# Optimization experiments

Measured on AMD Instinct MI355X. Metric: run time of the kernel, lower is better.

The kernel has to match this reference:

```python
import math
import jax, jax.numpy as jnp
import numpy as np

B, CIN, Hh, Ww = 8, 3, 64, 64
D_MODEL = 512
N_STATE = 64
N2 = N_STATE // 2
N_LAYERS = 4
LATENT = 256
L = Hh * Ww  # 4096
EPS = 1e-5


def setup_inputs() -> dict:
    key = jax.random.key(0)
    ks = jax.random.split(key, 12)
    x = jax.random.normal(ks[0], (B, CIN, Hh, Ww), jnp.float32)
    Wproj = jax.random.normal(ks[1], (D_MODEL, CIN), jnp.float32) * (1.0 / math.sqrt(CIN))
    bproj = jnp.zeros((D_MODEL,), jnp.float32)
    pos_emb = jax.random.normal(ks[2], (1, L, D_MODEL), jnp.float32)
    # S4D kernel params (stacked over layers), per minimal S4D init
    log_dt = jax.random.uniform(ks[3], (N_LAYERS, D_MODEL), jnp.float32) * (math.log(0.1) - math.log(0.001)) + math.log(0.001)
    log_A_real = jnp.full((N_LAYERS, D_MODEL, N2), math.log(0.5), jnp.float32)
    A_imag = jnp.broadcast_to(math.pi * jnp.arange(N2, dtype=jnp.float32), (N_LAYERS, D_MODEL, N2)) + jnp.zeros((N_LAYERS, D_MODEL, N2), jnp.float32)
    C_re = jax.random.normal(ks[4], (N_LAYERS, D_MODEL, N2), jnp.float32) * (0.5 ** 0.5)
    C_im = jax.random.normal(ks[5], (N_LAYERS, D_MODEL, N2), jnp.float32) * (0.5 ** 0.5)
    Dskip = jax.random.normal(ks[6], (N_LAYERS, D_MODEL), jnp.float32)
    Wout = jax.random.normal(ks[7], (N_LAYERS, 2 * D_MODEL, D_MODEL), jnp.float32) * (1.0 / math.sqrt(D_MODEL))
    bout = jnp.zeros((N_LAYERS, 2 * D_MODEL), jnp.float32)
    ln_g = jnp.ones((N_LAYERS, D_MODEL), jnp.float32)
    ln_b = jnp.zeros((N_LAYERS, D_MODEL), jnp.float32)
    Wstats = jax.random.normal(ks[8], (2 * LATENT, D_MODEL), jnp.float32) * (1.0 / math.sqrt(D_MODEL))
    bstats = jnp.zeros((2 * LATENT,), jnp.float32)
    return dict(x=x, Wproj=Wproj, bproj=bproj, pos_emb=pos_emb, log_dt=log_dt,
                log_A_real=log_A_real, A_imag=A_imag, C_re=C_re, C_im=C_im,
                Dskip=Dskip, Wout=Wout, bout=bout, ln_g=ln_g, ln_b=ln_b,
                Wstats=Wstats, bstats=bstats)


def _s4d_layer(u, log_dt, log_A_real, A_imag, C_re, C_im, Dskip, Wout, bout):
    # u: (B, H, L); diagonal SSM via Vandermonde kernel + FFT conv (minimal S4D)
    Lseq = u.shape[-1]
    dt = jnp.exp(log_dt)                              # (H,)
    A = -jnp.exp(log_A_real) + 1j * A_imag            # (H, N2)
    dtA = A * dt[:, None]                             # (H, N2)
    Cc = (C_re + 1j * C_im) * (jnp.exp(dtA) - 1.0) / A
    t = jnp.arange(Lseq, dtype=jnp.float32)
    K = 2.0 * jnp.einsum('hn,hnl->hl', Cc, jnp.exp(dtA[:, :, None] * t)).real  # (H, L)
    k_f = jnp.fft.rfft(K, n=2 * Lseq)                 # (H, L+1)
    u_f = jnp.fft.rfft(u, n=2 * Lseq)                 # (B, H, L+1)
    y = jnp.fft.irfft(u_f * k_f, n=2 * Lseq)[..., :Lseq]
    y = y + u * Dskip[:, None]
    y = jax.nn.gelu(y, approximate=False)
    # 1x1 conv to 2H then GLU over channel dim
    y2 = jnp.einsum('oh,bhl->bol', Wout, y) + bout[:, None]
    a, b = jnp.split(y2, 2, axis=1)
    return a * jax.nn.sigmoid(b)


def _layernorm(x, g, b):
    # x: (B, L, H), normalize over H
    mu = jnp.mean(x, axis=-1, keepdims=True)
    var = jnp.mean((x - mu) ** 2, axis=-1, keepdims=True)
    return (x - mu) * jax.lax.rsqrt(var + EPS) * g + b


def reference(x, Wproj, bproj, pos_emb, log_dt, log_A_real, A_imag, C_re, C_im,
              Dskip, Wout, bout, ln_g, ln_b, Wstats, bstats):
    Bx = x.shape[0]
    # 1x1 Conv2d input projection
    h = jnp.einsum('oc,bchw->bohw', Wproj, x) + bproj[None, :, None, None]
    h = h.reshape(Bx, D_MODEL, L).transpose(0, 2, 1)  # (B, L, D)
    h = h + pos_emb
    h = h.transpose(0, 2, 1)                          # (B, D, L)
    for i in range(N_LAYERS):
        z = _s4d_layer(h, log_dt[i], log_A_real[i], A_imag[i], C_re[i], C_im[i],
                       Dskip[i], Wout[i], bout[i])
        h = h + z                                     # residual (dropout = identity at eval)
        h = _layernorm(h.transpose(0, 2, 1), ln_g[i], ln_b[i]).transpose(0, 2, 1)
    h = h.mean(-1)                                    # (B, D)
    stats = h @ Wstats.T + bstats
    mu, log_sig = jnp.split(stats, 2, axis=-1)
    return mu, log_sig
```

## Files before the change

### kernel.cpp

```cpp
#include <hip/hip_runtime.h>
#include <hip/hip_bf16.h>
#include <hip/hip_fp16.h>
#include <cmath>

#define BATCH   8
#define D_MODEL 512
#define N2      32
#define LSEQ    4096
#define NLAYERS 4
#define CIN     3
#define NBDL    (16777216u)
#define PN      (D_MODEL * N2)
#define WN      (2 * D_MODEL * D_MODEL)

typedef __attribute__((ext_vector_type(8))) short short8;
typedef __attribute__((ext_vector_type(4))) float floatx4;

__device__ float   g_h[NBDL];
__device__ __align__(16) __hip_bfloat16 g_yb[NBDL];
__device__ __align__(16) __hip_bfloat16 g_yt[NBDL];
__device__ __align__(16) __hip_bfloat16 g_wb[NLAYERS * WN];
__device__ __align__(16) __hip_bfloat16 g_G[(size_t)NLAYERS * 512 * 6 * 4096];
__device__ float4  g_p[NLAYERS * PN];
__device__ float   g_hm[BATCH * D_MODEL];
__device__ int     g_flag;

__device__ __forceinline__ float bfbits2f(unsigned short u) {
    union { unsigned int i; float f; } x; x.i = ((unsigned int)u) << 16; return x.f;
}
__device__ __forceinline__ float halfbits2f(unsigned short u) {
    __half h; *(unsigned short*)&h = u; return __half2float(h);
}
__device__ __forceinline__ float ldin(const void* p, size_t i, int m) {
    if (m == 1) return ((const float*)p)[i];
    unsigned short u = ((const unsigned short*)p)[i];
    if (m == 0) return bfbits2f(u);
    return halfbits2f(u);
}
__device__ __forceinline__ unsigned int pk2(float a, float b) {
    __hip_bfloat16 ha = __float2bfloat16(a), hb = __float2bfloat16(b);
    unsigned short ua, ub;
    __builtin_memcpy(&ua, &ha, 2); __builtin_memcpy(&ub, &hb, 2);
    return (unsigned int)ua | ((unsigned int)ub << 16);
}
__device__ __forceinline__ void split2(float a, float b, unsigned int& hp, unsigned int& lp) {
    __hip_bfloat16 ah = __float2bfloat16(a), bh = __float2bfloat16(b);
    unsigned short ua, ub;
    __builtin_memcpy(&ua, &ah, 2); __builtin_memcpy(&ub, &bh, 2);
    hp = (unsigned int)ua | ((unsigned int)ub << 16);
    lp = pk2(a - __bfloat162float(ah), b - __bfloat162float(bh));
}
__device__ __forceinline__ float2 cpow_(float br, float bi, int e) {
    float rr = 1.f, ri = 0.f;
    while (e) {
        if (e & 1) { float t = rr * br - ri * bi; ri = rr * bi + ri * br; rr = t; }
        float t = br * br - bi * bi; bi = 2.f * br * bi; br = t;
        e >>= 1;
    }
    return make_float2(rr, ri);
}

__device__ __forceinline__ float fast_gelu(float x) {
    float z = x * 0.70710678118654752f;
    float a = fabsf(z);
    float t = __builtin_amdgcn_rcpf(fmaf(0.3275911f, a, 1.0f));
    float p = t * fmaf(t, fmaf(t, fmaf(t, fmaf(t, 1.061405429f, -1.453152027f),
                                       1.421413741f), -0.284496736f), 0.254829592f);
    float e = __expf(-a * a);
    float er = fmaf(-p, e, 1.0f);
    er = copysignf(er, z);
    float hx = 0.5f * x;
    return fmaf(hx, er, hx);
}

__global__ void detect_kernel(const unsigned short* a) {
    if (threadIdx.x == 0) {
        unsigned short h1 = a[1], h3 = a[3];
        int f;
        if (h1 == 0x0000 && h3 == 0x4049) f = 1;
        else if (h1 == 0x4049)            f = 0;
        else if (h1 == 0x4248)            f = 2;
        else                              f = 1;
        g_flag = f;
    }
}

__global__ __launch_bounds__(256) void sentinel_kernel(float* out, float v) {
    out[blockIdx.x * 256 + threadIdx.x] = v;
}

__global__ __launch_bounds__(256) void proj_kernel(const void* x, const void* Wproj,
                                                   const void* bproj, const void* pos) {
    const int m = g_flag;
    unsigned idx = blockIdx.x * 256 + threadIdx.x;
    int l = idx & (LSEQ - 1);
    int o = (idx >> 12) & (D_MODEL - 1);
    int b = idx >> 21;
    float acc = ldin(bproj, o, m) + ldin(pos, (size_t)l * D_MODEL + o, m);
#pragma unroll
    for (int c = 0; c < CIN; c++)
        acc = fmaf(ldin(Wproj, o * CIN + c, m),
                   ldin(x, (size_t)(b * CIN + c) * LSEQ + l, m), acc);
    g_h[idx] = acc;
}

__global__ __launch_bounds__(256) void prep_kernel(const void* log_dt, const void* log_A_real,
                                                   const void* A_imag, const void* C_re,
                                                   const void* C_im) {
    const int m = g_flag;
    int idx = blockIdx.x * 256 + threadIdx.x;
    int layer = idx >> 14;
    int i = idx & (PN - 1);
    int hh = i >> 5;
    size_t oH = (size_t)layer * D_MODEL;
    size_t oN = (size_t)layer * PN;
    float dt  = expf(ldin(log_dt, oH + hh, m));
    float a   = expf(ldin(log_A_real, oN + i, m));
    float bi  = ldin(A_imag, oN + i, m);
    float dre = -a * dt, dim = bi * dt;
    float er  = expf(dre);
    float wr  = er * cosf(dim);
    float wi  = er * sinf(dim);
    float Er  = wr - 1.0f, Ei = wi;
    float inv = 1.0f / (a * a + bi * bi);
    float Tr = (-Er * a + Ei * bi) * inv;
    float Ti = -(Er * bi + Ei * a) * inv;
    float cr = ldin(C_re, oN + i, m), ci = ldin(C_im, oN + i, m);
    float c2r = 2.0f * (cr * Tr - ci * Ti);
    float c2i = 2.0f * (cr * Ti + ci * Tr);
    g_p[idx] = make_float4(wr, wi, c2r, c2i);
}

__global__ __launch_bounds__(256) void pack_w_kernel(const void* Wout) {
    int idx = blockIdx.x * 256 + threadIdx.x;
    g_wb[idx] = __float2bfloat16(ldin(Wout, idx, g_flag));
}

__global__ __launch_bounds__(256) void gmat_kernel() {
    __shared__ float4 psh[32];
    __shared__ float Ksh[64];
    int tid = threadIdx.x;
    int bid = blockIdx.x;
    int layer = bid >> 9, h = bid & 511;
    if (tid < 32) psh[tid] = g_p[(size_t)layer * PN + h * N2 + tid];
    __syncthreads();
    if (tid < 64) {
        float acc = 0.f;
        for (int n = 0; n < 32; n++) {
            float4 pv = psh[n];
            float2 wd = cpow_(pv.x, pv.y, tid);
            acc = fmaf(pv.z, wd.x, fmaf(-pv.w, wd.y, acc));
        }
        Ksh[tid] = acc;
    }
    __syncthreads();
    __hip_bfloat16* G = g_G + (size_t)bid * 6 * 4096;
    for (int e = tid; e < 4096; e += 256) {
        int t = e >> 6, j = e & 63;
        float kv = (t >= j) ? Ksh[t - j] : 0.f;
        __hip_bfloat16 khi = __float2bfloat16(kv);
        G[e] = khi;
        G[4096 + e] = __float2bfloat16(kv - __bfloat162float(khi));
        {
            int n = t >> 1;
            float4 pv = psh[n];
            float2 wd = cpow_(pv.x, pv.y, 63 - j);
            float av = (t & 1) ? wd.y : wd.x;
            __hip_bfloat16 ahi = __float2bfloat16(av);
            G[2 * 4096 + e] = ahi;
            G[3 * 4096 + e] = __float2bfloat16(av - __bfloat162float(ahi));
        }
        {
            int n = j >> 1;
            float4 pv = psh[n];
            float2 wd = cpow_(pv.x, pv.y, t + 1);
            float zr = pv.z * wd.x - pv.w * wd.y;
            float zi = pv.z * wd.y + pv.w * wd.x;
            float cv = (j & 1) ? -zi : zr;
            __hip_bfloat16 chi = __float2bfloat16(cv);
            G[4 * 4096 + e] = chi;
            G[5 * 4096 + e] = __float2bfloat16(cv - __bfloat162float(chi));
        }
    }
}

__global__ __launch_bounds__(256) void ssd_kernel(const void* Dskip, int layer) {
    __shared__ unsigned short sMhi[64][72];
    __shared__ unsigned short sMlo[64][72];
    __shared__ unsigned short sAC[64][72];
    __shared__ unsigned short sUhi[64][72];
    __shared__ unsigned short sUlo[64][72];
    __shared__ float sPf[64][68];
    const int m = g_flag;
    int tid = threadIdx.x;
    int bid = blockIdx.x;
    int h = bid >> 3, b = bid & 7;
    const unsigned short* Gsrc = (const unsigned short*)g_G + (size_t)(layer * 512 + h) * 6 * 4096;

    {
        int row = tid >> 2, seg = (tid & 3) * 16;
        const unsigned short* s = Gsrc + row * 64 + seg;
        *(uint4*)&sMhi[row][seg]     = *(const uint4*)(s);
        *(uint4*)&sMhi[row][seg + 8] = *(const uint4*)(s + 8);
        *(uint4*)&sMlo[row][seg]     = *(const uint4*)(s + 4096);
        *(uint4*)&sMlo[row][seg + 8] = *(const uint4*)(s + 4096 + 8);
        *(uint4*)&sAC[row][seg]      = *(const uint4*)(s + 2 * 4096);
        *(uint4*)&sAC[row][seg + 8]  = *(const uint4*)(s + 2 * 4096 + 8);
    }
    {
        const float* ub = g_h + (size_t)(b * D_MODEL + h) * LSEQ;
        int c = tid >> 2, j0 = (tid & 3) * 16;
        const float* up = ub + c * 64 + j0;
#pragma unroll
        for (int s8 = 0; s8 < 2; s8++) {
            float4 va = *(const float4*)(up + s8 * 8);
            float4 vb = *(const float4*)(up + s8 * 8 + 4);
            uint4 H, L;
            split2(va.x, va.y, H.x, L.x);
            split2(va.z, va.w, H.y, L.y);
            split2(vb.x, vb.y, H.z, L.z);
            split2(vb.z, vb.w, H.w, L.w);
            *(uint4*)&sUhi[c][j0 + s8 * 8] = H;
            *(uint4*)&sUlo[c][j0 + s8 * 8] = L;
        }
    }
    __syncthreads();

    int lane = tid & 63, wave = tid >> 6;
    int q = lane >> 4, nm = lane & 15;
    int cidx = wave * 16 + nm;
    floatx4 zed = {0.f, 0.f, 0.f, 0.f};
    floatx4 pacc[4] = {zed, zed, zed, zed};

#pragma unroll
    for (int k0 = 0; k0 < 64; k0 += 32) {
        short8 bh = *(short8*)&sUhi[cidx][k0 + q * 8];
        short8 bl = *(short8*)&sUlo[cidx][k0 + q * 8];
#pragma unroll
        for (int mi = 0; mi < 4; mi++) {
            short8 a = *(short8*)&sAC[mi * 16 + nm][k0 + q * 8];
            pacc[mi] = __builtin_amdgcn_mfma_f32_16x16x32_bf16(a, bh, pacc[mi], 0, 0, 0);
            pacc[mi] = __builtin_amdgcn_mfma_f32_16x16x32_bf16(a, bl, pacc[mi], 0, 0, 0);
        }
    }
    __syncthreads();
    if (tid >= 128) {
        int idx = tid - 128, row = idx >> 1, seg = (idx & 1) * 32;
        const unsigned short* s = Gsrc + 3 * 4096 + row * 64 + seg;
        *(uint4*)&sAC[row][seg]      = *(const uint4*)(s);
        *(uint4*)&sAC[row][seg + 8]  = *(const uint4*)(s + 8);
        *(uint4*)&sAC[row][seg + 16] = *(const uint4*)(s + 16);
        *(uint4*)&sAC[row][seg + 24] = *(const uint4*)(s + 24);
    }
    __syncthreads();
#pragma unroll
    for (int k0 = 0; k0 < 64; k0 += 32) {
        short8 bh = *(short8*)&sUhi[cidx][k0 + q * 8];
#pragma unroll
        for (int mi = 0; mi < 4; mi++) {
            short8 a = *(short8*)&sAC[mi * 16 + nm][k0 + q * 8];
            pacc[mi] = __builtin_amdgcn_mfma_f32_16x16x32_bf16(a, bh, pacc[mi], 0, 0, 0);
        }
    }
#pragma unroll
    for (int mi = 0; mi < 4; mi++)
        *(floatx4*)&sPf[cidx][mi * 16 + q * 4] = pacc[mi];
    __syncthreads();

    if (tid < 32) {
        int n = tid;
        float4 pv = g_p[(size_t)layer * PN + h * N2 + n];
        float Wr = pv.x, Wi = pv.y;
#pragma unroll
        for (int s6 = 0; s6 < 6; s6++) { float t2 = Wr * Wr - Wi * Wi; Wi = 2.f * Wr * Wi; Wr = t2; }
        float Sr = 0.f, Si = 0.f;
        for (int c = 0; c < 64; c++) {
            unsigned int* wp = (unsigned int*)&sPf[c][0];
            unsigned int pru = wp[2 * n], piu = wp[2 * n + 1];
            float pr = __uint_as_float(pru), pi = __uint_as_float(piu);
            unsigned int shw, slw;
            split2(Sr, Si, shw, slw);
            wp[n]      = shw;
            wp[32 + n] = slw;
            float t2 = fmaf(Wr, Sr, fmaf(-Wi, Si, pr));
            Si = fmaf(Wr, Si, fmaf(Wi, Sr, pi));
            Sr = t2;
        }
    }
    if (tid >= 128) {
        int idx = tid - 128, row = idx >> 1, seg = (idx & 1) * 32;
        const unsigned short* s = Gsrc + 4 * 4096 + row * 64 + seg;
        *(uint4*)&sAC[row][seg]      = *(const uint4*)(s);
        *(uint4*)&sAC[row][seg + 8]  = *(const uint4*)(s + 8);
        *(uint4*)&sAC[row][seg + 16] = *(const uint4*)(s + 16);
        *(uint4*)&sAC[row][seg + 24] = *(const uint4*)(s + 24);
    }
    __syncthreads();

    floatx4 accA[4] = {zed, zed, zed, zed};
    floatx4 accB[4] = {zed, zed, zed, zed};
#pragma unroll
    for (int k0 = 0; k0 < 64; k0 += 32) {
        short8 bh = *(short8*)&sUhi[cidx][k0 + q * 8];
        short8 bl = *(short8*)&sUlo[cidx][k0 + q * 8];
        const unsigned short* srow = (const unsigned short*)&sPf[cidx][0];
        short8 sh = *(short8*)(srow + k0 + q * 8);
        short8 sl = *(short8*)(srow + 64 + k0 + q * 8);
#pragma unroll
        for (int mi = 0; mi < 4; mi++) {
            short8 amh = *(short8*)&sMhi[mi * 16 + nm][k0 + q * 8];
            short8 aml = *(short8*)&sMlo[mi * 16 + nm][k0 + q * 8];
            short8 ac  = *(short8*)&sAC [mi * 16 + nm][k0 + q * 8];
            accA[mi] = __builtin_amdgcn_mfma_f32_16x16x32_bf16(amh, bh, accA[mi], 0, 0, 0);
            accA[mi] = __builtin_amdgcn_mfma_f32_16x16x32_bf16(amh, bl, accA[mi], 0, 0, 0);
            accA[mi] = __builtin_amdgcn_mfma_f32_16x16x32_bf16(aml, bh, accA[mi], 0, 0, 0);
            accB[mi] = __builtin_amdgcn_mfma_f32_16x16x32_bf16(ac,  sh, accB[mi], 0, 0, 0);
            accB[mi] = __builtin_amdgcn_mfma_f32_16x16x32_bf16(ac,  sl, accB[mi], 0, 0, 0);
        }
    }
    __syncthreads();
    if (tid >= 128) {
        int idx = tid - 128, row = idx >> 1, seg = (idx & 1) * 32;
        const unsigned short* s = Gsrc + 5 * 4096 + row * 64 + seg;
        *(uint4*)&sAC[row][seg]      = *(const uint4*)(s);
        *(uint4*)&sAC[row][seg + 8]  = *(const uint4*)(s + 8);
        *(uint4*)&sAC[row][seg + 16] = *(const uint4*)(s + 16);
        *(uint4*)&sAC[row][seg + 24] = *(const uint4*)(s + 24);
    }
    __syncthreads();
#pragma unroll
    for (int k0 = 0; k0 < 64; k0 += 32) {
        const unsigned short* srow = (const unsigned short*)&sPf[cidx][0];
        short8 sh = *(short8*)(srow + k0 + q * 8);
#pragma unroll
        for (int mi = 0; mi < 4; mi++) {
            short8 ac = *(short8*)&sAC[mi * 16 + nm][k0 + q * 8];
            accB[mi] = __builtin_amdgcn_mfma_f32_16x16x32_bf16(ac, sh, accB[mi], 0, 0, 0);
        }
    }

    float dsk = ldin(Dskip, (size_t)layer * D_MODEL + h, m);
    __hip_bfloat16* yb = g_yb + (size_t)(b * D_MODEL + h) * LSEQ;
#pragma unroll
    for (int mi = 0; mi < 4; mi++) {
        int t0 = mi * 16 + q * 4;
        uint2 uh = *(uint2*)&sUhi[cidx][t0];
        uint2 ul = *(uint2*)&sUlo[cidx][t0];
        float u0 = bfbits2f((unsigned short)(uh.x & 0xFFFF)) + bfbits2f((unsigned short)(ul.x & 0xFFFF));
        float u1 = bfbits2f((unsigned short)(uh.x >> 16))    + bfbits2f((unsigned short)(ul.x >> 16));
        float u2 = bfbits2f((unsigned short)(uh.y & 0xFFFF)) + bfbits2f((unsigned short)(ul.y & 0xFFFF));
        float u3 = bfbits2f((unsigned short)(uh.y >> 16))    + bfbits2f((unsigned short)(ul.y >> 16));
        float y0 = fast_gelu(accA[mi][0] + accB[mi][0] + dsk * u0);
        float y1 = fast_gelu(accA[mi][1] + accB[mi][1] + dsk * u1);
        float y2 = fast_gelu(accA[mi][2] + accB[mi][2] + dsk * u2);
        float y3 = fast_gelu(accA[mi][3] + accB[mi][3] + dsk * u3);
        uint2 o;
        o.x = pk2(y0, y1);
        o.y = pk2(y2, y3);
        *(uint2*)&yb[cidx * 64 + t0] = o;
    }
}

__global__ __launch_bounds__(256, 4) void glu_mfma_kernel(const void* bout, int layer) {
    __shared__ __align__(16) unsigned char smem[25600];
    unsigned short (* __restrict__ Wa)[40] = (unsigned short(*)[40])(smem);
    unsigned short (* __restrict__ Wb)[40] = (unsigned short(*)[40])(smem + 2560);
    unsigned int*  __restrict__ Ytd        = (unsigned int*)(smem + 5120);
    unsigned short (* __restrict__ Zs)[264] = (unsigned short(*)[264])(smem);
    const int m = g_flag;
    int tid  = threadIdx.x;
    int wave = tid >> 6, lane = tid & 63;
    int q = lane >> 4, nm = lane & 15;
    int bid = blockIdx.x;
    int xcd = bid & 7;
    int qb  = bid >> 3;
    int rt  = qb & 15;
    int ct  = (xcd << 4) | (qb >> 4);
    int col0 = ct * 256;
    int row0 = rt * 32;
    int b  = col0 >> 12;
    int l0 = col0 & (LSEQ - 1);
    const unsigned short* __restrict__ Ybb =
        (const unsigned short*)g_yb + (size_t)b * D_MODEL * LSEQ;
    const __hip_bfloat16* __restrict__ Wbase = g_wb + (size_t)layer * WN;

    floatx4 accA[2][4], accB[2][4];
    floatx4 zed = {0.f, 0.f, 0.f, 0.f};
#pragma unroll
    for (int i = 0; i < 2; i++)
#pragma unroll
        for (int j = 0; j < 4; j++) { accA[i][j] = zed; accB[i][j] = zed; }

    int sk = (tid & 3) * 8;
    int wrow = (tid & 127) >> 2;
    int p  = tid >> 4;
    int sg = tid & 15;
    int Xw = (sg & 3) << 2;
    unsigned int rowbase = (unsigned)(sg * 16) * 20 + (unsigned)(p ^ Xw);
    int wavecol = wave * 64;

    for (int k0 = 0; k0 < D_MODEL; k0 += 32) {
        if (tid < 128)
            *(uint4*)&Wa[wrow][sk] = *(const uint4*)&Wbase[(size_t)(row0 + wrow) * D_MODEL + k0 + sk];
        else
            *(uint4*)&Wb[wrow][sk] = *(const uint4*)&Wbase[(size_t)(row0 + wrow + D_MODEL) * D_MODEL + k0 + sk];
        {
            const unsigned short* yA = Ybb + (size_t)(k0 + 2 * p) * LSEQ + l0 + sg * 16;
            uint4 a0 = *(const uint4*)yA;
            uint4 a1 = *(const uint4*)(yA + 8);
            uint4 b0 = *(const uint4*)(yA + LSEQ);
            uint4 b1 = *(const uint4*)(yA + LSEQ + 8);
#define PKW(au, bu, jj)  { \
            Ytd[rowbase + (jj) * 20]       = ((au) & 0xFFFFu) | ((bu) << 16); \
            Ytd[rowbase + ((jj) + 1) * 20] = ((au) >> 16) | ((bu) & 0xFFFF0000u); }
            PKW(a0.x, b0.x, 0)  PKW(a0.y, b0.y, 2)  PKW(a0.z, b0.z, 4)  PKW(a0.w, b0.w, 6)
            PKW(a1.x, b1.x, 8)  PKW(a1.y, b1.y, 10) PKW(a1.z, b1.z, 12) PKW(a1.w, b1.w, 14)
#undef PKW
        }
        __syncthreads();
        short8 afa[2], afb[2];
#pragma unroll
        for (int mi = 0; mi < 2; mi++) {
            afa[mi] = *(short8*)&Wa[mi * 16 + nm][q * 8];
            afb[mi] = *(short8*)&Wb[mi * 16 + nm][q * 8];
        }
#pragma unroll
        for (int ni = 0; ni < 4; ni++) {
            int r = wavecol + ni * 16 + nm;
            int Xr = ((r >> 4) & 3) << 2;
            short8 bf = *(short8*)(Ytd + r * 20 + ((q * 4) ^ Xr));
#pragma unroll
            for (int mi = 0; mi < 2; mi++) {
                accA[mi][ni] = __builtin_amdgcn_mfma_f32_16x16x32_bf16(afa[mi], bf, accA[mi][ni], 0, 0, 0);
                accB[mi][ni] = __builtin_amdgcn_mfma_f32_16x16x32_bf16(afb[mi], bf, accB[mi][ni], 0, 0, 0);
            }
        }
        __syncthreads();
    }

    size_t boff = (size_t)layer * 2 * D_MODEL;
#pragma unroll
    for (int mi = 0; mi < 2; mi++) {
#pragma unroll
        for (int r = 0; r < 4; r++) {
            int lrow = mi * 16 + q * 4 + r;
            int o = row0 + lrow;
            float ba  = ldin(bout, boff + o, m);
            float bb2 = ldin(bout, boff + o + D_MODEL, m);
#pragma unroll
            for (int ni = 0; ni < 4; ni++) {
                int lcol = wavecol + ni * 16 + nm;
                float aa = accA[mi][ni][r] + ba;
                float bv = accB[mi][ni][r] + bb2;
                float z  = aa * __builtin_amdgcn_rcpf(1.0f + __expf(-bv));
                __half hz = __float2half(z);
                unsigned short hzb;
                __builtin_memcpy(&hzb, &hz, 2);
                Zs[lrow][lcol] = hzb;
            }
        }
    }
    __syncthreads();
    unsigned short* __restrict__ Zb =
        (unsigned short*)g_yt + (size_t)b * D_MODEL * LSEQ;
    int zrow = tid >> 3;
    int zcol = (tid & 7) * 32;
    size_t gbase = (size_t)(row0 + zrow) * LSEQ + l0 + zcol;
#pragma unroll
    for (int i = 0; i < 4; i++)
        *(uint4*)&Zb[gbase + i * 8] = *(uint4*)&Zs[zrow][zcol + i * 8];
}

__global__ __launch_bounds__(256) void ln_kernel(const void* g, const void* bt, int layer) {
    __shared__ float s_sum[8][32];
    __shared__ float s_sq[8][32];
    __shared__ float s_mu[32], s_rs[32];
    const int m = g_flag;
    int tid = threadIdx.x;
    int l  = tid & 31;
    int dg = tid >> 5;
    int bl = blockIdx.x;
    int b  = bl >> 7;
    int l0 = (bl & 127) * 32;
    size_t base = (size_t)b * D_MODEL * LSEQ + l0 + l;
    float* __restrict__ hp = g_h + base + (size_t)(dg * 64) * LSEQ;
    const unsigned short* __restrict__ zp =
        (const unsigned short*)g_yt + base + (size_t)(dg * 64) * LSEQ;
    size_t goff = (size_t)layer * D_MODEL + dg * 64;
    float varr[64];
    float sum = 0.f, sq = 0.f;
#pragma unroll
    for (int i = 0; i < 64; i++) {
        float v = hp[(size_t)i * LSEQ] + halfbits2f(zp[(size_t)i * LSEQ]);
        varr[i] = v;
        sum += v; sq += v * v;
    }
    s_sum[dg][l] = sum; s_sq[dg][l] = sq;
    __syncthreads();
    if (tid < 32) {
        float s = 0.f, qq = 0.f;
#pragma unroll
        for (int gq = 0; gq < 8; gq++) { s += s_sum[gq][tid]; qq += s_sq[gq][tid]; }
        float mu = s * (1.0f / D_MODEL);
        float var = qq * (1.0f / D_MODEL) - mu * mu;
        s_mu[tid] = mu;
        s_rs[tid] = rsqrtf(var + 1e-5f);
    }
    __syncthreads();
    float mu = s_mu[l], rs = s_rs[l];
#pragma unroll
    for (int i = 0; i < 64; i++) {
        hp[(size_t)i * LSEQ] = (varr[i] - mu) * rs * ldin(g, goff + i, m) + ldin(bt, goff + i, m);
    }
}

__global__ __launch_bounds__(256) void mean_kernel() {
    int bd = blockIdx.x;
    int tid = threadIdx.x;
    const float* __restrict__ row = g_h + (size_t)bd * LSEQ;
    float s = 0.f;
    for (int l = tid; l < LSEQ; l += 256) s += row[l];
#pragma unroll
    for (int off = 32; off > 0; off >>= 1) s += __shfl_down(s, off, 64);
    __shared__ float red[4];
    if ((tid & 63) == 0) red[tid >> 6] = s;
    __syncthreads();
    if (tid == 0) g_hm[bd] = (red[0] + red[1] + red[2] + red[3]) * (1.0f / LSEQ);
}

__global__ __launch_bounds__(256) void stats_kernel(const void* Wst, const void* bst,
                                                    float* __restrict__ out) {
    const int m = g_flag;
    int idx = blockIdx.x * 256 + threadIdx.x;
    int b = idx >> 9, o = idx & (D_MODEL - 1);
    const float* __restrict__ hb = g_hm + b * D_MODEL;
    float acc = ldin(bst, o, m);
    for (int d = 0; d < D_MODEL; d++)
        acc = fmaf(hb[d], ldin(Wst, (size_t)o * D_MODEL + d, m), acc);
    int pos = (o < 256) ? (b * 256 + o) : (2048 + b * 256 + (o - 256));
    out[pos] = acc;
}

extern "C" void kernel_launch(void* const* d_in, const int* in_sizes, int n_in,
                              void* d_out, int out_size, void* d_ws, size_t ws_size,
                              hipStream_t stream) {
    static const int exp_sizes[16] = {98304, 1536, 512, 2097152, 2048, 65536, 65536,
                                      65536, 65536, 2048, 2097152, 4096, 2048, 2048,
                                      262144, 512};
    bool ok = (n_in == 16);
    if (ok) for (int i = 0; i < 16; i++) if (in_sizes[i] != exp_sizes[i]) { ok = false; break; }
    if (!ok) {
        sentinel_kernel<<<(out_size + 255) / 256, 256, 0, stream>>>((float*)d_out, 1000.0f);
        return;
    }
    if (out_size != 4096) {
        sentinel_kernel<<<(out_size + 255) / 256, 256, 0, stream>>>((float*)d_out, 300.0f);
        return;
    }

    const void* x          = d_in[0];
    const void* Wproj      = d_in[1];
    const void* bproj      = d_in[2];
    const void* pos        = d_in[3];
    const void* log_dt     = d_in[4];
    const void* log_A_real = d_in[5];
    const void* A_imag     = d_in[6];
    const void* C_re       = d_in[7];
    const void* C_im       = d_in[8];
    const void* Dskip      = d_in[9];
    const void* Wout       = d_in[10];
    const void* bout       = d_in[11];
    const void* ln_g       = d_in[12];
    const void* ln_b       = d_in[13];
    const void* Wstats     = d_in[14];
    const void* bstats     = d_in[15];

    detect_kernel<<<1, 64, 0, stream>>>((const unsigned short*)A_imag);
    proj_kernel<<<NBDL / 256, 256, 0, stream>>>(x, Wproj, bproj, pos);
    prep_kernel<<<(NLAYERS * PN) / 256, 256, 0, stream>>>(
        log_dt, log_A_real, A_imag, C_re, C_im);
    pack_w_kernel<<<(NLAYERS * WN) / 256, 256, 0, stream>>>(Wout);
    gmat_kernel<<<NLAYERS * 512, 256, 0, stream>>>();

    for (int i = 0; i < NLAYERS; i++) {
        ssd_kernel<<<BATCH * D_MODEL, 256, 0, stream>>>(Dskip, i);
        glu_mfma_kernel<<<2048, 256, 0, stream>>>(bout, i);
        ln_kernel<<<(BATCH * LSEQ) / 32, 256, 0, stream>>>(ln_g, ln_b, i);
    }

    mean_kernel<<<BATCH * D_MODEL, 256, 0, stream>>>();
    stats_kernel<<<(BATCH * D_MODEL) / 256, 256, 0, stream>>>(
        Wstats, bstats, (float*)d_out);
}
```

Baseline: 1.113 ms.

## Rewrite gmat kernel with incremental complex powers and vectorized stores; remap SSD blocks

Each gmat thread now computes a 16-element run with a single cpow_ call followed by repeated complex multiplication, replacing a binary-exponentiation call per element. The kernel K is built from per-mode partial sums staged in shared memory. The G matrices are written with 16-byte vector stores, and the transposed C block goes through shared memory so its global stores stay coalesced. The SSD block index mapping changes to h = bid & 511, b = bid >> 9, so consecutive blocks now take different heads; this alters how G reads hit the cache. Building powers by repeated multiplication accumulates a little more rounding error than direct exponentiation.

```diff
diff --git a/kernel.cpp b/kernel.cpp
--- a/kernel.cpp
+++ b/kernel.cpp
@@ -49,6 +49,10 @@
     __builtin_memcpy(&ua, &ah, 2); __builtin_memcpy(&ub, &bh, 2);
     hp = (unsigned int)ua | ((unsigned int)ub << 16);
     lp = pk2(a - __bfloat162float(ah), b - __bfloat162float(bh));
+}
+__device__ __forceinline__ unsigned short bf16u(float a) {
+    __hip_bfloat16 h = __float2bfloat16(a);
+    unsigned short u; __builtin_memcpy(&u, &h, 2); return u;
 }
 __device__ __forceinline__ float2 cpow_(float br, float bi, int e) {
     float rr = 1.f, ri = 0.f;
@@ -138,50 +142,110 @@
 
 __global__ __launch_bounds__(256) void gmat_kernel() {
     __shared__ float4 psh[32];
-    __shared__ float Ksh[64];
+    __shared__ unsigned short Khi[64], Klo[64];
+    __shared__ __align__(16) unsigned short sC[2][64][72];
+    float (*Kpart)[64] = (float(*)[64])&sC[0][0][0];
     int tid = threadIdx.x;
     int bid = blockIdx.x;
     int layer = bid >> 9, h = bid & 511;
     if (tid < 32) psh[tid] = g_p[(size_t)layer * PN + h * N2 + tid];
     __syncthreads();
+    if (tid < 128) {
+        int n = tid >> 2, dseg = (tid & 3) * 16;
+        float4 pv = psh[n];
+        float wr = pv.x, wi = pv.y;
+        float2 wd = cpow_(wr, wi, dseg);
+#pragma unroll
+        for (int i = 0; i < 16; i++) {
+            Kpart[n][dseg + i] = pv.z * wd.x - pv.w * wd.y;
+            float t2 = wd.x * wr - wd.y * wi;
+            wd.y = wd.x * wi + wd.y * wr; wd.x = t2;
+        }
+    }
+    __syncthreads();
     if (tid < 64) {
         float acc = 0.f;
-        for (int n = 0; n < 32; n++) {
-            float4 pv = psh[n];
-            float2 wd = cpow_(pv.x, pv.y, tid);
-            acc = fmaf(pv.z, wd.x, fmaf(-pv.w, wd.y, acc));
-        }
-        Ksh[tid] = acc;
-    }
-    __syncthreads();
-    __hip_bfloat16* G = g_G + (size_t)bid * 6 * 4096;
-    for (int e = tid; e < 4096; e += 256) {
-        int t = e >> 6, j = e & 63;
-        float kv = (t >= j) ? Ksh[t - j] : 0.f;
-        __hip_bfloat16 khi = __float2bfloat16(kv);
-        G[e] = khi;
-        G[4096 + e] = __float2bfloat16(kv - __bfloat162float(khi));
-        {
-            int n = t >> 1;
-            float4 pv = psh[n];
-            float2 wd = cpow_(pv.x, pv.y, 63 - j);
-            float av = (t & 1) ? wd.y : wd.x;
-            __hip_bfloat16 ahi = __float2bfloat16(av);
-            G[2 * 4096 + e] = ahi;
-            G[3 * 4096 + e] = __float2bfloat16(av - __bfloat162float(ahi));
-        }
-        {
-            int n = j >> 1;
-            float4 pv = psh[n];
-            float2 wd = cpow_(pv.x, pv.y, t + 1);
+#pragma unroll
+        for (int n = 0; n < 32; n++) acc += Kpart[n][tid];
+        unsigned short khu = bf16u(acc);
+        Khi[tid] = khu;
+        Klo[tid] = bf16u(acc - bfbits2f(khu));
+    }
+    __syncthreads();
+    unsigned short* Gu = (unsigned short*)(g_G + (size_t)bid * 6 * 4096);
+    int t = tid >> 2, jseg = (tid & 3) * 16;
+    {
+        unsigned int mh[8], ml[8];
+#pragma unroll
+        for (int i2 = 0; i2 < 8; i2++) {
+            int d0 = t - jseg - 2 * i2;
+            int d1 = d0 - 1;
+            unsigned int h0 = (d0 >= 0) ? (unsigned int)Khi[d0] : 0u;
+            unsigned int h1 = (d1 >= 0) ? (unsigned int)Khi[d1] : 0u;
+            unsigned int l0v = (d0 >= 0) ? (unsigned int)Klo[d0] : 0u;
+            unsigned int l1v = (d1 >= 0) ? (unsigned int)Klo[d1] : 0u;
+            mh[i2] = h0 | (h1 << 16);
+            ml[i2] = l0v | (l1v << 16);
+        }
+        uint4 v;
+        v.x = mh[0]; v.y = mh[1]; v.z = mh[2]; v.w = mh[3];
+        *(uint4*)&Gu[t * 64 + jseg] = v;
+        v.x = mh[4]; v.y = mh[5]; v.z = mh[6]; v.w = mh[7];
+        *(uint4*)&Gu[t * 64 + jseg + 8] = v;
+        v.x = ml[0]; v.y = ml[1]; v.z = ml[2]; v.w = ml[3];
+        *(uint4*)&Gu[4096 + t * 64 + jseg] = v;
+        v.x = ml[4]; v.y = ml[5]; v.z = ml[6]; v.w = ml[7];
+        *(uint4*)&Gu[4096 + t * 64 + jseg + 8] = v;
+    }
+    {
+        int n = t >> 1;
+        float4 pv = psh[n];
+        float wr = pv.x, wi = pv.y;
+        float av[16];
+        float2 wd = cpow_(wr, wi, 48 - jseg);
+#pragma unroll
+        for (int i = 15; i >= 0; i--) {
+            av[i] = (t & 1) ? wd.y : wd.x;
+            float t2 = wd.x * wr - wd.y * wi;
+            wd.y = wd.x * wi + wd.y * wr; wd.x = t2;
+        }
+        unsigned int ah[8], al[8];
+#pragma unroll
+        for (int i2 = 0; i2 < 8; i2++)
+            split2(av[2 * i2], av[2 * i2 + 1], ah[i2], al[i2]);
+        uint4 v;
+        v.x = ah[0]; v.y = ah[1]; v.z = ah[2]; v.w = ah[3];
+        *(uint4*)&Gu[2 * 4096 + t * 64 + jseg] = v;
+        v.x = ah[4]; v.y = ah[5]; v.z = ah[6]; v.w = ah[7];
+        *(uint4*)&Gu[2 * 4096 + t * 64 + jseg + 8] = v;
+        v.x = al[0]; v.y = al[1]; v.z = al[2]; v.w = al[3];
+        *(uint4*)&Gu[3 * 4096 + t * 64 + jseg] = v;
+        v.x = al[4]; v.y = al[5]; v.z = al[6]; v.w = al[7];
+        *(uint4*)&Gu[3 * 4096 + t * 64 + jseg + 8] = v;
+    }
+    {
+        int j = tid >> 2, tseg = (tid & 3) * 16;
+        int n = j >> 1;
+        float4 pv = psh[n];
+        float wr = pv.x, wi = pv.y;
+        float2 wd = cpow_(wr, wi, tseg + 1);
+#pragma unroll
+        for (int i = 0; i < 16; i++) {
             float zr = pv.z * wd.x - pv.w * wd.y;
             float zi = pv.z * wd.y + pv.w * wd.x;
             float cv = (j & 1) ? -zi : zr;
-            __hip_bfloat16 chi = __float2bfloat16(cv);
-            G[4 * 4096 + e] = chi;
-            G[5 * 4096 + e] = __float2bfloat16(cv - __bfloat162float(chi));
-        }
-    }
+            unsigned short chu = bf16u(cv);
+            sC[0][tseg + i][j] = chu;
+            sC[1][tseg + i][j] = bf16u(cv - bfbits2f(chu));
+            float t2 = wd.x * wr - wd.y * wi;
+            wd.y = wd.x * wi + wd.y * wr; wd.x = t2;
+        }
+    }
+    __syncthreads();
+    *(uint4*)&Gu[4 * 4096 + t * 64 + jseg]     = *(uint4*)&sC[0][t][jseg];
+    *(uint4*)&Gu[4 * 4096 + t * 64 + jseg + 8] = *(uint4*)&sC[0][t][jseg + 8];
+    *(uint4*)&Gu[5 * 4096 + t * 64 + jseg]     = *(uint4*)&sC[1][t][jseg];
+    *(uint4*)&Gu[5 * 4096 + t * 64 + jseg + 8] = *(uint4*)&sC[1][t][jseg + 8];
 }
 
 __global__ __launch_bounds__(256) void ssd_kernel(const void* Dskip, int layer) {
@@ -194,7 +258,7 @@
     const int m = g_flag;
     int tid = threadIdx.x;
     int bid = blockIdx.x;
-    int h = bid >> 3, b = bid & 7;
+    int h = bid & 511, b = bid >> 9;
     const unsigned short* Gsrc = (const unsigned short*)g_G + (size_t)(layer * 512 + h) * 6 * 4096;
 
     {
```

New measurement: 1.050 ms. -5.6%, faster.
